# Kernel optimization log

Hardware: AMD Instinct MI355X
Metric: run time of the kernel (lower is better)

## Reference

```python
import jax, jax.numpy as jnp
import numpy as np

N_NODES = 50000
N_EDGES = 800000
NDIM_IN = 64
EDIM = 64
HID = 152  # size_embedding
NDIM_OUT = 64


def _linear(x, W, b):
    # torch nn.Linear: y = x @ W.T + b
    return jnp.matmul(x, W.T) + b


def _sage_layer(nf, ef, Wm, bm, Wa, ba, src, dst):
    # message: gather src node feats, concat edge feats, linear -> [E,1,F]
    m = _linear(jnp.concatenate([nf[src], ef], axis=2), Wm, bm)
    # mean scatter-reduce to dst nodes (zero for nodes with no in-edges)
    s = jax.ops.segment_sum(m, dst, num_segments=N_NODES)
    deg = jax.ops.segment_sum(jnp.ones((m.shape[0],), m.dtype), dst, num_segments=N_NODES)
    h_neigh = s / jnp.maximum(deg, 1.0)[:, None, None]
    # update: concat self + neighbor agg, linear, relu
    return jax.nn.relu(_linear(jnp.concatenate([nf, h_neigh], axis=2), Wa, ba))


def setup_inputs() -> dict:
    key = jax.random.key(0)
    ks = jax.random.split(key, 16)
    def lin_params(kw, kb, fan_in, fan_out):
        bound = 1.0 / np.sqrt(fan_in)
        W = jax.random.uniform(kw, (fan_out, fan_in), jnp.float32, -bound, bound)
        b = jax.random.uniform(kb, (fan_out,), jnp.float32, -bound, bound)
        return W, b
    nfeats = jax.random.normal(ks[0], (N_NODES, 1, NDIM_IN), jnp.float32)
    efeats = jax.random.normal(ks[1], (N_EDGES, 1, EDIM), jnp.float32)
    src = jax.random.randint(ks[2], (N_EDGES,), 0, N_NODES, jnp.int32)
    dst = jax.random.randint(ks[3], (N_EDGES,), 0, N_NODES, jnp.int32)
    Wm1, bm1 = lin_params(ks[4], ks[5], NDIM_IN + EDIM, HID)
    Wa1, ba1 = lin_params(ks[6], ks[7], NDIM_IN + HID, HID)
    Wm2, bm2 = lin_params(ks[8], ks[9], HID + EDIM, HID)
    Wa2, ba2 = lin_params(ks[10], ks[11], HID + HID, HID)
    Wm3, bm3 = lin_params(ks[12], ks[13], HID + EDIM, NDIM_OUT)
    Wa3, ba3 = lin_params(ks[14], ks[15], HID + NDIM_OUT, NDIM_OUT)
    return {
        "nfeats": nfeats, "efeats": efeats,
        "Wm1": Wm1, "bm1": bm1, "Wa1": Wa1, "ba1": ba1,
        "Wm2": Wm2, "bm2": bm2, "Wa2": Wa2, "ba2": ba2,
        "Wm3": Wm3, "bm3": bm3, "Wa3": Wa3, "ba3": ba3,
        "src": src, "dst": dst,
    }


def reference(nfeats, efeats, Wm1, bm1, Wa1, ba1, Wm2, bm2, Wa2, ba2,
              Wm3, bm3, Wa3, ba3, src, dst):
    # dropout is identity in eval mode
    h = _sage_layer(nfeats, efeats, Wm1, bm1, Wa1, ba1, src, dst)
    h = _sage_layer(h, efeats, Wm2, bm2, Wa2, ba2, src, dst)
    h = _sage_layer(h, efeats, Wm3, bm3, Wa3, ba3, src, dst)
    return h.sum(axis=1)  # [N, ndim_out]
```

## Files before the change

### kernel.cpp

```cpp
#include <hip/hip_runtime.h>


#define NN 50000
#define NE 800000
#define NIN 64
#define EDIM_ 64
#define HID_ 152
#define NOUT 64
#define PADN 50176

__global__ __launch_bounds__(256) void hist_kernel(const int* __restrict__ dst,
                                                   int* __restrict__ ideg) {
    int e = blockIdx.x * 256 + threadIdx.x;
    if (e < NE) atomicAdd(&ideg[dst[e]], 1);
}

__global__ __launch_bounds__(256) void scan1_kernel(const int* __restrict__ in,
                                                    int* __restrict__ out,
                                                    int* __restrict__ bsum) {
    __shared__ int ws[4];
    int t = threadIdx.x;
    int base = blockIdx.x * 1024 + t * 4;
    int a0 = in[base], a1 = in[base + 1], a2 = in[base + 2], a3 = in[base + 3];
    int s = a0 + a1 + a2 + a3;
    int lane = t & 63, wid = t >> 6;
    int v = s;
#pragma unroll
    for (int d = 1; d < 64; d <<= 1) {
        int u = __shfl_up(v, d);
        if (lane >= d) v += u;
    }
    if (lane == 63) ws[wid] = v;
    __syncthreads();
    int wofs = 0;
    if (wid > 0) wofs += ws[0];
    if (wid > 1) wofs += ws[1];
    if (wid > 2) wofs += ws[2];
    int excl = wofs + v - s;
    out[base] = excl;
    out[base + 1] = excl + a0;
    out[base + 2] = excl + a0 + a1;
    out[base + 3] = excl + a0 + a1 + a2;
    if (t == 255) bsum[blockIdx.x] = wofs + v;
}

__global__ __launch_bounds__(64) void scan2_kernel(int* __restrict__ bsum, int nb) {
    int t = threadIdx.x;
    int orig = (t < nb) ? bsum[t] : 0;
    int v = orig;
#pragma unroll
    for (int d = 1; d < 64; d <<= 1) {
        int u = __shfl_up(v, d);
        if (t >= d) v += u;
    }
    if (t < nb) bsum[t] = v - orig;
}

__global__ __launch_bounds__(256) void scan3_kernel(int* __restrict__ out,
                                                    const int* __restrict__ bsum) {
    int base = blockIdx.x * 1024 + threadIdx.x * 4;
    int b = bsum[blockIdx.x];
    out[base] += b; out[base + 1] += b; out[base + 2] += b; out[base + 3] += b;
}

__global__ __launch_bounds__(256) void scatter_edges_kernel(const int* __restrict__ src,
                                                            const int* __restrict__ dst,
                                                            int* __restrict__ cursor,
                                                            int* __restrict__ csr_nf,
                                                            int* __restrict__ csr_ef) {
    int e = blockIdx.x * 256 + threadIdx.x;
    if (e >= NE) return;
    int d = dst[e];
    int pos = atomicAdd(&cursor[d], 1);
    csr_nf[pos] = src[e];
    csr_ef[pos] = e;
}

template <int F>
__global__ __launch_bounds__(256) void agg_kernel(const float* __restrict__ table,
                                                  const int* __restrict__ rows,
                                                  const int* __restrict__ off,
                                                  float* __restrict__ out) {
    constexpr int C = F / 8;
    constexpr int NPW = 64 / C;
    int t = threadIdx.x;
    int lane = t & 63, wid = t >> 6;
    int sub = lane / C;
    int ch = lane - sub * C;
    int n = (blockIdx.x * 4 + wid) * NPW + sub;
    if (sub >= NPW || n >= NN) return;
    int s = off[n], e = off[n + 1];
    float4 a0 = {0,0,0,0}, a1 = {0,0,0,0}, b0 = {0,0,0,0}, b1 = {0,0,0,0};
    int i = s;
    for (; i + 1 < e; i += 2) {
        const float* p0 = table + (size_t)rows[i] * F + ch * 8;
        const float* p1 = table + (size_t)rows[i + 1] * F + ch * 8;
        float4 u0 = *(const float4*)p0;
        float4 u1 = *(const float4*)(p0 + 4);
        float4 v0 = *(const float4*)p1;
        float4 v1 = *(const float4*)(p1 + 4);
        a0.x += u0.x; a0.y += u0.y; a0.z += u0.z; a0.w += u0.w;
        a1.x += u1.x; a1.y += u1.y; a1.z += u1.z; a1.w += u1.w;
        b0.x += v0.x; b0.y += v0.y; b0.z += v0.z; b0.w += v0.w;
        b1.x += v1.x; b1.y += v1.y; b1.z += v1.z; b1.w += v1.w;
    }
    if (i < e) {
        const float* p0 = table + (size_t)rows[i] * F + ch * 8;
        float4 u0 = *(const float4*)p0;
        float4 u1 = *(const float4*)(p0 + 4);
        a0.x += u0.x; a0.y += u0.y; a0.z += u0.z; a0.w += u0.w;
        a1.x += u1.x; a1.y += u1.y; a1.z += u1.z; a1.w += u1.w;
    }
    float4 r0, r1;
    r0.x = a0.x + b0.x; r0.y = a0.y + b0.y; r0.z = a0.z + b0.z; r0.w = a0.w + b0.w;
    r1.x = a1.x + b1.x; r1.y = a1.y + b1.y; r1.z = a1.z + b1.z; r1.w = a1.w + b1.w;
    float* o = out + (size_t)n * F + ch * 8;
    *(float4*)o = r0;
    *(float4*)(o + 4) = r1;
}

template <int K1, int K2, int NT, bool MSG>
__global__ __launch_bounds__(256) void gemm_kernel(const float* __restrict__ X1,
                                                   const float* __restrict__ X2,
                                                   const float* __restrict__ W,
                                                   const float* __restrict__ bias,
                                                   const int* __restrict__ off,
                                                   float* __restrict__ out) {
    constexpr int KT = K1 + K2;
    __shared__ float Xs[8][132];
    __shared__ float Ws[8][68];
    const int t = threadIdx.x;
    const int m0 = blockIdx.x * 128;
    const int n0 = blockIdx.y * 64;
    const int xrow = t >> 1;
    const int xk = (t & 1) * 4;
    const int wrow = t >> 2;
    const int wk = (t & 3) * 2;
    const int tx = t & 15;
    const int ty = t >> 4;
    float acc[8][4] = {};

    const bool xrow_ok = (m0 + xrow) < NN;
    const bool wrow_ok = (n0 + wrow) < NT;

#pragma unroll
    for (int seg = 0; seg < 2; ++seg) {
        const float* __restrict__ X = seg ? X2 : X1;
        const int K = seg ? K2 : K1;
        const int koff = seg ? K1 : 0;
        for (int k0 = 0; k0 < K; k0 += 8) {
            float4 xv = make_float4(0.f, 0.f, 0.f, 0.f);
            if (xrow_ok) xv = *(const float4*)(X + (size_t)(m0 + xrow) * K + k0 + xk);
            float2 wv = make_float2(0.f, 0.f);
            if (wrow_ok) wv = *(const float2*)(W + (size_t)(n0 + wrow) * KT + koff + k0 + wk);
            __syncthreads();
            Xs[xk][xrow] = xv.x; Xs[xk + 1][xrow] = xv.y;
            Xs[xk + 2][xrow] = xv.z; Xs[xk + 3][xrow] = xv.w;
            Ws[wk][wrow] = wv.x; Ws[wk + 1][wrow] = wv.y;
            __syncthreads();
#pragma unroll
            for (int k = 0; k < 8; ++k) {
                float4 a0 = *(const float4*)&Xs[k][ty * 8];
                float4 a1 = *(const float4*)&Xs[k][ty * 8 + 4];
                float4 b = *(const float4*)&Ws[k][tx * 4];
                acc[0][0] += a0.x * b.x; acc[0][1] += a0.x * b.y; acc[0][2] += a0.x * b.z; acc[0][3] += a0.x * b.w;
                acc[1][0] += a0.y * b.x; acc[1][1] += a0.y * b.y; acc[1][2] += a0.y * b.z; acc[1][3] += a0.y * b.w;
                acc[2][0] += a0.z * b.x; acc[2][1] += a0.z * b.y; acc[2][2] += a0.z * b.z; acc[2][3] += a0.z * b.w;
                acc[3][0] += a0.w * b.x; acc[3][1] += a0.w * b.y; acc[3][2] += a0.w * b.z; acc[3][3] += a0.w * b.w;
                acc[4][0] += a1.x * b.x; acc[4][1] += a1.x * b.y; acc[4][2] += a1.x * b.z; acc[4][3] += a1.x * b.w;
                acc[5][0] += a1.y * b.x; acc[5][1] += a1.y * b.y; acc[5][2] += a1.y * b.z; acc[5][3] += a1.y * b.w;
                acc[6][0] += a1.z * b.x; acc[6][1] += a1.z * b.y; acc[6][2] += a1.z * b.z; acc[6][3] += a1.z * b.w;
                acc[7][0] += a1.w * b.x; acc[7][1] += a1.w * b.y; acc[7][2] += a1.w * b.z; acc[7][3] += a1.w * b.w;
            }
        }
    }

    const int o0 = n0 + tx * 4;
    if (o0 >= NT) return;
    float b0 = bias[o0], b1 = bias[o0 + 1], b2 = bias[o0 + 2], b3 = bias[o0 + 3];
#pragma unroll
    for (int i = 0; i < 8; ++i) {
        int n = m0 + ty * 8 + i;
        if (n >= NN) break;
        float4 r;
        if (MSG) {
            float d = (float)(off[n + 1] - off[n]);
            float inv = 1.0f / fmaxf(d, 1.0f);
            r.x = (acc[i][0] + d * b0) * inv;
            r.y = (acc[i][1] + d * b1) * inv;
            r.z = (acc[i][2] + d * b2) * inv;
            r.w = (acc[i][3] + d * b3) * inv;
        } else {
            r.x = fmaxf(acc[i][0] + b0, 0.0f);
            r.y = fmaxf(acc[i][1] + b1, 0.0f);
            r.z = fmaxf(acc[i][2] + b2, 0.0f);
            r.w = fmaxf(acc[i][3] + b3, 0.0f);
        }
        *(float4*)(out + (size_t)n * NT + o0) = r;
    }
}

extern "C" void kernel_launch(void* const* d_in, const int* in_sizes, int n_in,
                              void* d_out, int out_size, void* d_ws, size_t ws_size,
                              hipStream_t stream) {
    const float* nfeats = (const float*)d_in[0];
    const float* efeats = (const float*)d_in[1];
    const float* Wm1 = (const float*)d_in[2];
    const float* bm1 = (const float*)d_in[3];
    const float* Wa1 = (const float*)d_in[4];
    const float* ba1 = (const float*)d_in[5];
    const float* Wm2 = (const float*)d_in[6];
    const float* bm2 = (const float*)d_in[7];
    const float* Wa2 = (const float*)d_in[8];
    const float* ba2 = (const float*)d_in[9];
    const float* Wm3 = (const float*)d_in[10];
    const float* bm3 = (const float*)d_in[11];
    const float* Wa3 = (const float*)d_in[12];
    const float* ba3 = (const float*)d_in[13];
    const int* src = (const int*)d_in[14];
    const int* dst = (const int*)d_in[15];
    float* out = (float*)d_out;

    int* iws = (int*)d_ws;
    int* ideg   = iws;
    int* off    = iws + PADN;
    int* cursor = iws + 2 * PADN;
    int* csr_nf = iws + 3 * PADN;
    int* csr_ef = csr_nf + NE;
    float* B = (float*)(csr_ef + NE);
    float* P = B + 3200000;
    float* Q = P + 7600000;
    float* R = Q + 7600000;

    const int BLK = 256;
    auto cdiv = [](long long a, long long b) { return (int)((a + b - 1) / b); };
    dim3 g152(cdiv(NN, 128), cdiv(152, 64));
    dim3 g64(cdiv(NN, 128), 1);
    const int NB = PADN / 1024;

    hipMemsetAsync(ideg, 0, (size_t)PADN * 4, stream);
    hist_kernel<<<cdiv(NE, BLK), BLK, 0, stream>>>(dst, ideg);
    scan1_kernel<<<NB, 256, 0, stream>>>(ideg, off, cursor);
    scan2_kernel<<<1, 64, 0, stream>>>(cursor, NB);
    scan3_kernel<<<NB, 256, 0, stream>>>(off, cursor);
    hipMemcpyAsync(cursor, off, (size_t)NN * 4, hipMemcpyDeviceToDevice, stream);
    scatter_edges_kernel<<<cdiv(NE, BLK), BLK, 0, stream>>>(src, dst, cursor, csr_nf, csr_ef);

    agg_kernel<EDIM_><<<cdiv(NN, 32), BLK, 0, stream>>>(efeats, csr_ef, off, B);

    agg_kernel<NIN><<<cdiv(NN, 32), BLK, 0, stream>>>(nfeats, csr_nf, off, P);
    gemm_kernel<NIN, EDIM_, HID_, true><<<g152, BLK, 0, stream>>>(P, B, Wm1, bm1, off, Q);
    gemm_kernel<NIN, HID_, HID_, false><<<g152, BLK, 0, stream>>>(nfeats, Q, Wa1, ba1, off, R);

    agg_kernel<HID_><<<cdiv(NN, 12), BLK, 0, stream>>>(R, csr_nf, off, P);
    gemm_kernel<HID_, EDIM_, HID_, true><<<g152, BLK, 0, stream>>>(P, B, Wm2, bm2, off, Q);
    gemm_kernel<HID_, HID_, HID_, false><<<g152, BLK, 0, stream>>>(R, Q, Wa2, ba2, off, P);

    agg_kernel<HID_><<<cdiv(NN, 12), BLK, 0, stream>>>(P, csr_nf, off, Q);
    gemm_kernel<HID_, EDIM_, NOUT, true><<<g64, BLK, 0, stream>>>(Q, B, Wm3, bm3, off, R);
    gemm_kernel<HID_, NOUT, NOUT, false><<<g64, BLK, 0, stream>>>(P, R, Wa3, ba3, off, out);
}
```

Baseline: 923.6 us.

## Double-buffer GEMM tiles with K=16 and pad hidden feature rows to 160

The GEMM kernel now uses a K-tile of 16 with two shared-memory buffers. It prefetches the next tile into registers while computing the current one, which halves the barrier count per K step. Hidden-feature buffers use a padded row stride of 160 floats so K can be padded to multiples of 16. This adds wasted reads of pad columns in the X loads (garbage multiplied by zeroed weights) and doubles shared-memory use per block.

```diff
diff --git a/kernel.cpp b/kernel.cpp
--- a/kernel.cpp
+++ b/kernel.cpp
@@ -6,6 +6,7 @@
 #define NIN 64
 #define EDIM_ 64
 #define HID_ 152
+#define S152 160
 #define NOUT 64
 #define PADN 50176
 
@@ -76,7 +77,7 @@
     csr_ef[pos] = e;
 }
 
-template <int F>
+template <int F, int S>
 __global__ __launch_bounds__(256) void agg_kernel(const float* __restrict__ table,
                                                   const int* __restrict__ rows,
                                                   const int* __restrict__ off,
@@ -93,8 +94,8 @@
     float4 a0 = {0,0,0,0}, a1 = {0,0,0,0}, b0 = {0,0,0,0}, b1 = {0,0,0,0};
     int i = s;
     for (; i + 1 < e; i += 2) {
-        const float* p0 = table + (size_t)rows[i] * F + ch * 8;
-        const float* p1 = table + (size_t)rows[i + 1] * F + ch * 8;
+        const float* p0 = table + (size_t)rows[i] * S + ch * 8;
+        const float* p1 = table + (size_t)rows[i + 1] * S + ch * 8;
         float4 u0 = *(const float4*)p0;
         float4 u1 = *(const float4*)(p0 + 4);
         float4 v0 = *(const float4*)p1;
@@ -105,7 +106,7 @@
         b1.x += v1.x; b1.y += v1.y; b1.z += v1.z; b1.w += v1.w;
     }
     if (i < e) {
-        const float* p0 = table + (size_t)rows[i] * F + ch * 8;
+        const float* p0 = table + (size_t)rows[i] * S + ch * 8;
         float4 u0 = *(const float4*)p0;
         float4 u1 = *(const float4*)(p0 + 4);
         a0.x += u0.x; a0.y += u0.y; a0.z += u0.z; a0.w += u0.w;
@@ -114,12 +115,12 @@
     float4 r0, r1;
     r0.x = a0.x + b0.x; r0.y = a0.y + b0.y; r0.z = a0.z + b0.z; r0.w = a0.w + b0.w;
     r1.x = a1.x + b1.x; r1.y = a1.y + b1.y; r1.z = a1.z + b1.z; r1.w = a1.w + b1.w;
-    float* o = out + (size_t)n * F + ch * 8;
+    float* o = out + (size_t)n * S + ch * 8;
     *(float4*)o = r0;
     *(float4*)(o + 4) = r1;
 }
 
-template <int K1, int K2, int NT, bool MSG>
+template <int K1, int S1, int K2, int S2, int NT, int SOUT, bool MSG>
 __global__ __launch_bounds__(256) void gemm_kernel(const float* __restrict__ X1,
                                                    const float* __restrict__ X2,
                                                    const float* __restrict__ W,
@@ -127,15 +128,18 @@
                                                    const int* __restrict__ off,
                                                    float* __restrict__ out) {
     constexpr int KT = K1 + K2;
-    __shared__ float Xs[8][132];
-    __shared__ float Ws[8][68];
+    constexpr int K1P = (K1 + 15) & ~15;
+    constexpr int K2P = (K2 + 15) & ~15;
+    constexpr int NIT = (K1P + K2P) / 16;
+    __shared__ float Xs[2][16][132];
+    __shared__ float Ws[2][16][68];
     const int t = threadIdx.x;
     const int m0 = blockIdx.x * 128;
     const int n0 = blockIdx.y * 64;
     const int xrow = t >> 1;
-    const int xk = (t & 1) * 4;
+    const int xks = (t & 1) * 8;
     const int wrow = t >> 2;
-    const int wk = (t & 3) * 2;
+    const int wks = (t & 3) * 4;
     const int tx = t & 15;
     const int ty = t >> 4;
     float acc[8][4] = {};
@@ -143,36 +147,57 @@
     const bool xrow_ok = (m0 + xrow) < NN;
     const bool wrow_ok = (n0 + wrow) < NT;
 
-#pragma unroll
-    for (int seg = 0; seg < 2; ++seg) {
-        const float* __restrict__ X = seg ? X2 : X1;
-        const int K = seg ? K2 : K1;
-        const int koff = seg ? K1 : 0;
-        for (int k0 = 0; k0 < K; k0 += 8) {
-            float4 xv = make_float4(0.f, 0.f, 0.f, 0.f);
-            if (xrow_ok) xv = *(const float4*)(X + (size_t)(m0 + xrow) * K + k0 + xk);
-            float2 wv = make_float2(0.f, 0.f);
-            if (wrow_ok) wv = *(const float2*)(W + (size_t)(n0 + wrow) * KT + koff + k0 + wk);
-            __syncthreads();
-            Xs[xk][xrow] = xv.x; Xs[xk + 1][xrow] = xv.y;
-            Xs[xk + 2][xrow] = xv.z; Xs[xk + 3][xrow] = xv.w;
-            Ws[wk][wrow] = wv.x; Ws[wk + 1][wrow] = wv.y;
-            __syncthreads();
-#pragma unroll
-            for (int k = 0; k < 8; ++k) {
-                float4 a0 = *(const float4*)&Xs[k][ty * 8];
-                float4 a1 = *(const float4*)&Xs[k][ty * 8 + 4];
-                float4 b = *(const float4*)&Ws[k][tx * 4];
-                acc[0][0] += a0.x * b.x; acc[0][1] += a0.x * b.y; acc[0][2] += a0.x * b.z; acc[0][3] += a0.x * b.w;
-                acc[1][0] += a0.y * b.x; acc[1][1] += a0.y * b.y; acc[1][2] += a0.y * b.z; acc[1][3] += a0.y * b.w;
-                acc[2][0] += a0.z * b.x; acc[2][1] += a0.z * b.y; acc[2][2] += a0.z * b.z; acc[2][3] += a0.z * b.w;
-                acc[3][0] += a0.w * b.x; acc[3][1] += a0.w * b.y; acc[3][2] += a0.w * b.z; acc[3][3] += a0.w * b.w;
-                acc[4][0] += a1.x * b.x; acc[4][1] += a1.x * b.y; acc[4][2] += a1.x * b.z; acc[4][3] += a1.x * b.w;
-                acc[5][0] += a1.y * b.x; acc[5][1] += a1.y * b.y; acc[5][2] += a1.y * b.z; acc[5][3] += a1.y * b.w;
-                acc[6][0] += a1.z * b.x; acc[6][1] += a1.z * b.y; acc[6][2] += a1.z * b.z; acc[6][3] += a1.z * b.w;
-                acc[7][0] += a1.w * b.x; acc[7][1] += a1.w * b.y; acc[7][2] += a1.w * b.z; acc[7][3] += a1.w * b.w;
-            }
+    auto load_tile = [&](int it, float4& xa, float4& xb, float4& wv) {
+        const int it16 = it * 16;
+        const bool sg2 = (it16 >= K1P);
+        const float* __restrict__ X = sg2 ? X2 : X1;
+        const int S = sg2 ? S2 : S1;
+        const int Ka = sg2 ? K2 : K1;
+        const int koff = sg2 ? K1 : 0;
+        const int k0 = sg2 ? (it16 - K1P) : it16;
+        xa = make_float4(0.f, 0.f, 0.f, 0.f);
+        xb = xa; wv = xa;
+        if (xrow_ok) {
+            const float* p = X + (size_t)(m0 + xrow) * S + k0 + xks;
+            xa = *(const float4*)p;
+            xb = *(const float4*)(p + 4);
         }
+        const int kk = k0 + wks;
+        if (wrow_ok && kk < Ka)
+            wv = *(const float4*)(W + (size_t)(n0 + wrow) * KT + koff + kk);
+    };
+    auto store_tile = [&](int buf, const float4& xa, const float4& xb, const float4& wv) {
+        Xs[buf][xks + 0][xrow] = xa.x; Xs[buf][xks + 1][xrow] = xa.y;
+        Xs[buf][xks + 2][xrow] = xa.z; Xs[buf][xks + 3][xrow] = xa.w;
+        Xs[buf][xks + 4][xrow] = xb.x; Xs[buf][xks + 5][xrow] = xb.y;
+        Xs[buf][xks + 6][xrow] = xb.z; Xs[buf][xks + 7][xrow] = xb.w;
+        Ws[buf][wks + 0][wrow] = wv.x; Ws[buf][wks + 1][wrow] = wv.y;
+        Ws[buf][wks + 2][wrow] = wv.z; Ws[buf][wks + 3][wrow] = wv.w;
+    };
+
+    float4 xa, xb, wv;
+    load_tile(0, xa, xb, wv);
+    store_tile(0, xa, xb, wv);
+#pragma unroll 2
+    for (int it = 0; it < NIT; ++it) {
+        const int buf = it & 1;
+        __syncthreads();
+        if (it + 1 < NIT) load_tile(it + 1, xa, xb, wv);
+#pragma unroll
+        for (int k = 0; k < 16; ++k) {
+            float4 a0 = *(const float4*)&Xs[buf][k][ty * 8];
+            float4 a1 = *(const float4*)&Xs[buf][k][ty * 8 + 4];
+            float4 b  = *(const float4*)&Ws[buf][k][tx * 4];
+            acc[0][0] += a0.x * b.x; acc[0][1] += a0.x * b.y; acc[0][2] += a0.x * b.z; acc[0][3] += a0.x * b.w;
+            acc[1][0] += a0.y * b.x; acc[1][1] += a0.y * b.y; acc[1][2] += a0.y * b.z; acc[1][3] += a0.y * b.w;
+            acc[2][0] += a0.z * b.x; acc[2][1] += a0.z * b.y; acc[2][2] += a0.z * b.z; acc[2][3] += a0.z * b.w;
+            acc[3][0] += a0.w * b.x; acc[3][1] += a0.w * b.y; acc[3][2] += a0.w * b.z; acc[3][3] += a0.w * b.w;
+            acc[4][0] += a1.x * b.x; acc[4][1] += a1.x * b.y; acc[4][2] += a1.x * b.z; acc[4][3] += a1.x * b.w;
+            acc[5][0] += a1.y * b.x; acc[5][1] += a1.y * b.y; acc[5][2] += a1.y * b.z; acc[5][3] += a1.y * b.w;
+            acc[6][0] += a1.z * b.x; acc[6][1] += a1.z * b.y; acc[6][2] += a1.z * b.z; acc[6][3] += a1.z * b.w;
+            acc[7][0] += a1.w * b.x; acc[7][1] += a1.w * b.y; acc[7][2] += a1.w * b.z; acc[7][3] += a1.w * b.w;
+        }
+        if (it + 1 < NIT) store_tile(1 - buf, xa, xb, wv);
     }
 
     const int o0 = n0 + tx * 4;
@@ -196,7 +221,7 @@
             r.z = fmaxf(acc[i][2] + b2, 0.0f);
             r.w = fmaxf(acc[i][3] + b3, 0.0f);
         }
-        *(float4*)(out + (size_t)n * NT + o0) = r;
+        *(float4*)(out + (size_t)n * SOUT + o0) = r;
     }
 }
 
@@ -229,8 +254,8 @@
     int* csr_ef = csr_nf + NE;
     float* B = (float*)(csr_ef + NE);
     float* P = B + 3200000;
-    float* Q = P + 7600000;
-    float* R = Q + 7600000;
+    float* Q = P + (size_t)NN * S152;
+    float* R = Q + (size_t)NN * S152;
 
     const int BLK = 256;
     auto cdiv = [](long long a, long long b) { return (int)((a + b - 1) / b); };
@@ -246,17 +271,17 @@
     hipMemcpyAsync(cursor, off, (size_t)NN * 4, hipMemcpyDeviceToDevice, stream);
     scatter_edges_kernel<<<cdiv(NE, BLK), BLK, 0, stream>>>(src, dst, cursor, csr_nf, csr_ef);
 
-    agg_kernel<EDIM_><<<cdiv(NN, 32), BLK, 0, stream>>>(efeats, csr_ef, off, B);
-
-    agg_kernel<NIN><<<cdiv(NN, 32), BLK, 0, stream>>>(nfeats, csr_nf, off, P);
-    gemm_kernel<NIN, EDIM_, HID_, true><<<g152, BLK, 0, stream>>>(P, B, Wm1, bm1, off, Q);
-    gemm_kernel<NIN, HID_, HID_, false><<<g152, BLK, 0, stream>>>(nfeats, Q, Wa1, ba1, off, R);
-
-    agg_kernel<HID_><<<cdiv(NN, 12), BLK, 0, stream>>>(R, csr_nf, off, P);
-    gemm_kernel<HID_, EDIM_, HID_, true><<<g152, BLK, 0, stream>>>(P, B, Wm2, bm2, off, Q);
-    gemm_kernel<HID_, HID_, HID_, false><<<g152, BLK, 0, stream>>>(R, Q, Wa2, ba2, off, P);
-
-    agg_kernel<HID_><<<cdiv(NN, 12), BLK, 0, stream>>>(P, csr_nf, off, Q);
-    gemm_kernel<HID_, EDIM_, NOUT, true><<<g64, BLK, 0, stream>>>(Q, B, Wm3, bm3, off, R);
-    gemm_kernel<HID_, NOUT, NOUT, false><<<g64, BLK, 0, stream>>>(P, R, Wa3, ba3, off, out);
-}
+    agg_kernel<EDIM_, EDIM_><<<cdiv(NN, 32), BLK, 0, stream>>>(efeats, csr_ef, off, B);
+
+    agg_kernel<NIN, NIN><<<cdiv(NN, 32), BLK, 0, stream>>>(nfeats, csr_nf, off, P);
+    gemm_kernel<NIN, NIN, EDIM_, EDIM_, HID_, S152, true><<<g152, BLK, 0, stream>>>(P, B, Wm1, bm1, off, Q);
+    gemm_kernel<NIN, NIN, HID_, S152, HID_, S152, false><<<g152, BLK, 0, stream>>>(nfeats, Q, Wa1, ba1, off, R);
+
+    agg_kernel<HID_, S152><<<cdiv(NN, 12), BLK, 0, stream>>>(R, csr_nf, off, P);
+    gemm_kernel<HID_, S152, EDIM_, EDIM_, HID_, S152, true><<<g152, BLK, 0, stream>>>(P, B, Wm2, bm2, off, Q);
+    gemm_kernel<HID_, S152, HID_, S152, HID_, S152, false><<<g152, BLK, 0, stream>>>(R, Q, Wa2, ba2, off, P);
+
+    agg_kernel<HID_, S152><<<cdiv(NN, 12), BLK, 0, stream>>>(P, csr_nf, off, Q);
+    gemm_kernel<HID_, S152, EDIM_, EDIM_, NOUT, NOUT, true><<<g64, BLK, 0, stream>>>(Q, B, Wm3, bm3, off, R);
+    gemm_kernel<HID_, S152, NOUT, NOUT, NOUT, NOUT, false><<<g64, BLK, 0, stream>>>(P, R, Wa3, ba3, off, out);
+}
```

Result: slower. 1.144 ms (+23.8%).
